# Performance work log

Hardware: AMD Instinct MI355X
Metric: run time of the kernel (lower is better)

## Reference

```python
import jax, jax.numpy as jnp
import numpy as np

EPS = 1e-8  # torch cosine_similarity norm clamp

def _cos(a, b, axis=-1):
    na = jnp.maximum(jnp.linalg.norm(a, axis=axis), EPS)
    nb = jnp.maximum(jnp.linalg.norm(b, axis=axis), EPS)
    return jnp.sum(a * b, axis=axis) / (na * nb)

def setup_inputs() -> dict:
    key = jax.random.key(0)
    ks = jax.random.split(key, 9)
    B, L, D, S = 8, 8192, 512, 131072
    scale = 0.02
    x = jax.random.normal(ks[0], (B, L, D), jnp.float32)
    context_W = jax.random.normal(ks[1], (D, D), jnp.float32) * scale
    context_b = jnp.zeros((D,), jnp.float32)
    pred_W1 = jax.random.normal(ks[2], (D, D), jnp.float32) * scale
    pred_b1 = jnp.zeros((D,), jnp.float32)
    pred_W2 = jax.random.normal(ks[3], (D, D), jnp.float32) * scale
    pred_b2 = jnp.zeros((D,), jnp.float32)
    raw_embeddings = jax.random.normal(ks[4], (S, D), jnp.float32)
    u = jax.random.uniform(ks[5], (S,), jnp.float32)
    surprise_level = jnp.where(u > 0.5, u, 0.0)  # ~half the slots active
    return {"x": x, "context_W": context_W, "context_b": context_b,
            "pred_W1": pred_W1, "pred_b1": pred_b1,
            "pred_W2": pred_W2, "pred_b2": pred_b2,
            "raw_embeddings": raw_embeddings, "surprise_level": surprise_level}

def reference(x, context_W, context_b, pred_W1, pred_b1, pred_W2, pred_b2,
              raw_embeddings, surprise_level):
    # context = pad(x[:, :-1], left-shift by one along seq), i.e. causal previous token
    context = jnp.pad(x[:, :-1, :], ((0, 0), (1, 0), (0, 0)))
    # predictor MLP on projected context (torch Linear: y = x @ W.T + b)
    ctx = context @ context_W.T + context_b
    h = jax.nn.gelu(ctx @ pred_W1.T + pred_b1, approximate=False)
    prediction = h @ pred_W2.T + pred_b2  # [B, L, D]
    mse = jnp.mean((x - prediction) ** 2, axis=-1)
    prediction_surprise = jnp.sqrt(mse)  # [B, L]

    # memory-contrastive surprise: cosine sim of pooled x vs active stored embeddings
    active = surprise_level > 0  # [S]
    x_pooled = jnp.mean(x, axis=1)  # [B, D]
    sim = _cos(x_pooled[:, None, :], raw_embeddings[None, :, :])  # [B, S]
    sim = jnp.where(active[None, :], sim, -jnp.inf)
    max_sim = jnp.max(sim, axis=-1)           # [B]
    best_idx = jnp.argmax(sim, axis=-1)       # [B]
    best_stored = raw_embeddings[best_idx]    # [B, D] argmax-based gather
    divergence = 1.0 - _cos(x, best_stored[:, None, :])  # [B, L]
    pattern_match = (max_sim[:, None] > 0.3).astype(x.dtype)
    contrastive = pattern_match * divergence

    surprise = jnp.maximum(prediction_surprise, contrastive * 2.0)  # [B, L]
    return surprise
```

## Files before the change

### kernel.cpp

```cpp
#include <hip/hip_runtime.h>
#include <math.h>

#define OFF_SIMKEY   0
#define OFF_POOLED   1024
#define OFF_SSD      32768
#define OFF_NX2      294912
#define OFF_DOT      557056
#define ZEROED_BYTES 819200
#define OFF_MAXSIM   819200
#define OFF_NORME    819456
#define OFF_EBEST    819712
#define OFF_BPRIME   836608
#define OFF_WP       839680
#define OFF_W2B      1364992
#define OFF_H        1900544

typedef __attribute__((ext_vector_type(8))) short bf16x8;
typedef __attribute__((ext_vector_type(4))) float f32x4;

__device__ inline unsigned short f2bf(float f) {
    unsigned int u = __float_as_uint(f);
    unsigned int r = (u + 0x7FFFu + ((u >> 16) & 1u)) >> 16;
    return (unsigned short)r;
}

__device__ inline void load_lds_16(const void* g, void* l) {
    __builtin_amdgcn_global_load_lds((const __attribute__((address_space(1))) void*)g,
                                     (__attribute__((address_space(3))) void*)l, 16, 0, 0);
}

__global__ void __launch_bounds__(256) k_pre(const float* __restrict__ W1, const float* __restrict__ Wc,
                      const float* __restrict__ b1, const float* __restrict__ bc,
                      unsigned short* __restrict__ Wp, float* __restrict__ bprime) {
    __shared__ float w1s[8 * 512];
    int t = threadIdx.x;
    int n0 = blockIdx.x * 8;
    const float4* src = (const float4*)(W1 + (size_t)n0 * 512);
    float4* dst = (float4*)w1s;
#pragma unroll
    for (int c = 0; c < 4; ++c) dst[t + c * 256] = src[t + c * 256];
    __syncthreads();
    int k0 = t, k1 = t + 256;
    float acc0[8], acc1[8];
#pragma unroll
    for (int n = 0; n < 8; ++n) { acc0[n] = 0.f; acc1[n] = 0.f; }
    for (int j = 0; j < 512; ++j) {
        float a = Wc[(size_t)j * 512 + k0];
        float b = Wc[(size_t)j * 512 + k1];
#pragma unroll
        for (int n = 0; n < 8; ++n) {
            float w = w1s[n * 512 + j];
            acc0[n] += w * a; acc1[n] += w * b;
        }
    }
#pragma unroll
    for (int n = 0; n < 8; ++n) {
        Wp[(size_t)(n0 + n) * 512 + k0] = f2bf(acc0[n]);
        Wp[(size_t)(n0 + n) * 512 + k1] = f2bf(acc1[n]);
    }
    int nl = t >> 5, l32 = t & 31;
    float p = 0.f;
    for (int j = l32; j < 512; j += 32) p += w1s[nl * 512 + j] * bc[j];
#pragma unroll
    for (int m = 16; m >= 1; m >>= 1) p += __shfl_xor(p, m);
    if (l32 == 0) bprime[n0 + nl] = b1[n0 + nl] + p;
}

__global__ void __launch_bounds__(256) k_cast(const float* __restrict__ W2, unsigned short* __restrict__ W2b) {
    int i = blockIdx.x * 1024 + threadIdx.x * 4;
    float4 v = *(const float4*)(W2 + i);
    ushort4 o;
    o.x = f2bf(v.x); o.y = f2bf(v.y); o.z = f2bf(v.z); o.w = f2bf(v.w);
    *(ushort4*)(W2b + i) = o;
}

__global__ void __launch_bounds__(512) k_pool(const float* __restrict__ x, float* __restrict__ pooled) {
    int d = threadIdx.x;
    int b = blockIdx.y;
    int l0 = blockIdx.x * 128;
    const float* p = x + ((size_t)b * 8192 + l0) * 512 + d;
    float s = 0.f;
    for (int i = 0; i < 128; ++i) s += p[(size_t)i * 512];
    atomicAdd(&pooled[b * 512 + d], s);
}

__global__ void __launch_bounds__(256) k_sim(const float* __restrict__ E, const float* __restrict__ sl,
                     const float* __restrict__ pooledws, unsigned long long* __restrict__ simkey) {
    __shared__ float ps[4096];
    __shared__ unsigned long long wkey[4][8];
    int t = threadIdx.x, lane = t & 63, w = t >> 6;
#pragma unroll
    for (int c = 0; c < 16; ++c) ps[t + c * 256] = pooledws[t + c * 256] * (1.0f / 8192.0f);
    __syncthreads();
    float pr[8][8];
#pragma unroll
    for (int b = 0; b < 8; ++b) {
        float4 v0 = *(const float4*)&ps[b * 512 + lane * 8];
        float4 v1 = *(const float4*)&ps[b * 512 + lane * 8 + 4];
        pr[b][0] = v0.x; pr[b][1] = v0.y; pr[b][2] = v0.z; pr[b][3] = v0.w;
        pr[b][4] = v1.x; pr[b][5] = v1.y; pr[b][6] = v1.z; pr[b][7] = v1.w;
    }
    float npinv[8];
#pragma unroll
    for (int b = 0; b < 8; ++b) {
        float s = 0.f;
#pragma unroll
        for (int j = 0; j < 8; ++j) s += pr[b][j] * pr[b][j];
#pragma unroll
        for (int m = 32; m >= 1; m >>= 1) s += __shfl_xor(s, m);
        npinv[b] = 1.0f / fmaxf(sqrtf(s), 1e-8f);
    }
    unsigned long long best[8];
#pragma unroll
    for (int b = 0; b < 8; ++b) best[b] = 0ull;
    int sbase = blockIdx.x * 512 + w * 128;
    for (int g = 0; g < 2; ++g) {
        float mysl = sl[sbase + g * 64 + lane];
        unsigned long long mask = __ballot(mysl > 0.0f);
        for (int it = 0; it < 64; ++it) {
            if (!((mask >> it) & 1ull)) continue;
            int s = sbase + g * 64 + it;
            const float4* ep = (const float4*)(E + (size_t)s * 512);
            float4 e0 = ep[lane * 2], e1 = ep[lane * 2 + 1];
            float nrm = e0.x * e0.x + e0.y * e0.y + e0.z * e0.z + e0.w * e0.w
                      + e1.x * e1.x + e1.y * e1.y + e1.z * e1.z + e1.w * e1.w;
            float dt[8];
#pragma unroll
            for (int b = 0; b < 8; ++b)
                dt[b] = e0.x * pr[b][0] + e0.y * pr[b][1] + e0.z * pr[b][2] + e0.w * pr[b][3]
                      + e1.x * pr[b][4] + e1.y * pr[b][5] + e1.z * pr[b][6] + e1.w * pr[b][7];
#pragma unroll
            for (int m = 32; m >= 1; m >>= 1) {
                nrm += __shfl_xor(nrm, m);
#pragma unroll
                for (int b = 0; b < 8; ++b) dt[b] += __shfl_xor(dt[b], m);
            }
            float neinv = 1.0f / fmaxf(sqrtf(nrm), 1e-8f);
#pragma unroll
            for (int b = 0; b < 8; ++b) {
                float sim = dt[b] * npinv[b] * neinv;
                unsigned int u = __float_as_uint(sim);
                unsigned int k32 = (u & 0x80000000u) ? ~u : (u | 0x80000000u);
                unsigned long long key = ((unsigned long long)k32 << 32) | (unsigned int)(~(unsigned int)s);
                if (key > best[b]) best[b] = key;
            }
        }
    }
    if (lane == 0) {
#pragma unroll
        for (int b = 0; b < 8; ++b) wkey[w][b] = best[b];
    }
    __syncthreads();
    if (t < 8) {
        unsigned long long k = wkey[0][t];
#pragma unroll
        for (int w2 = 1; w2 < 4; ++w2) if (wkey[w2][t] > k) k = wkey[w2][t];
        if (k) atomicMax(&simkey[t], k);
    }
}

__global__ void __launch_bounds__(64) k_b2(const float* __restrict__ E, const unsigned long long* __restrict__ simkey,
                    float* __restrict__ max_sim, float* __restrict__ norm_e, float* __restrict__ ebest) {
    int b = blockIdx.x, lane = threadIdx.x;
    unsigned long long key = simkey[b];
    float ms; unsigned int idx;
    if (key == 0ull) { ms = -1e30f; idx = 0u; }
    else {
        unsigned int k32 = (unsigned int)(key >> 32);
        unsigned int u = (k32 & 0x80000000u) ? (k32 & 0x7FFFFFFFu) : ~k32;
        ms = __uint_as_float(u);
        idx = ~(unsigned int)(key & 0xFFFFFFFFull);
    }
    const float4* ep = (const float4*)(E + (size_t)idx * 512);
    float4 e0 = ep[lane * 2], e1 = ep[lane * 2 + 1];
    *(float4*)&ebest[b * 512 + lane * 8] = e0;
    *(float4*)&ebest[b * 512 + lane * 8 + 4] = e1;
    float s = e0.x * e0.x + e0.y * e0.y + e0.z * e0.z + e0.w * e0.w
            + e1.x * e1.x + e1.y * e1.y + e1.z * e1.z + e1.w * e1.w;
#pragma unroll
    for (int m = 32; m >= 1; m >>= 1) s += __shfl_xor(s, m);
    if (lane == 0) { max_sim[b] = ms; norm_e[b] = fmaxf(sqrtf(s), 1e-8f); }
}

__global__ void __launch_bounds__(256) k_gemm1(const float* __restrict__ x, const unsigned short* __restrict__ Wp,
                        const float* __restrict__ bprime, unsigned short* __restrict__ H) {
    __shared__ char smem[32768];
    unsigned short* As = (unsigned short*)smem;
    unsigned short* Bs = (unsigned short*)(smem + 8192);
    int t = threadIdx.x, lane = t & 63, w = t >> 6, l15 = lane & 15, quad = lane >> 4;
    int cb = blockIdx.x, rb = blockIdx.y;
    int wr = w >> 1, wc = w & 1;
    f32x4 acc[4][4];
#pragma unroll
    for (int i = 0; i < 4; ++i)
#pragma unroll
        for (int j = 0; j < 4; ++j) acc[i][j] = (f32x4){0.f, 0.f, 0.f, 0.f};
    const int gr0 = rb * 128;
    for (int kt = 0; kt < 16; ++kt) {
        __syncthreads();
#pragma unroll
        for (int c = 0; c < 4; ++c) {
            int u = c * 256 + t;
            int row = u >> 3, f4 = u & 7;
            int gr = gr0 + row;
            int l = gr & 8191;
            float4 v = make_float4(0.f, 0.f, 0.f, 0.f);
            if (l != 0) v = *(const float4*)(x + ((size_t)gr - 1) * 512 + kt * 32 + f4 * 4);
            ushort4 o;
            o.x = f2bf(v.x); o.y = f2bf(v.y); o.z = f2bf(v.z); o.w = f2bf(v.w);
            *(ushort4*)&As[row * 32 + f4 * 4] = o;
        }
#pragma unroll
        for (int c = 0; c < 2; ++c) {
            int q = w * 2 + c;
            int unit = q * 64 + lane;
            int row = unit >> 2, kb = unit & 3;
            const unsigned short* g = Wp + (size_t)(cb * 128 + row) * 512 + kt * 32 + kb * 8;
            load_lds_16(g, Bs + q * 512);
        }
        __syncthreads();
        bf16x8 af[4], bfr[4];
#pragma unroll
        for (int i = 0; i < 4; ++i)
            af[i] = *(const bf16x8*)&As[(wr * 64 + i * 16 + l15) * 32 + quad * 8];
#pragma unroll
        for (int j = 0; j < 4; ++j)
            bfr[j] = *(const bf16x8*)&Bs[(wc * 64 + j * 16 + l15) * 32 + quad * 8];
#pragma unroll
        for (int i = 0; i < 4; ++i)
#pragma unroll
            for (int j = 0; j < 4; ++j)
                acc[i][j] = __builtin_amdgcn_mfma_f32_16x16x32_bf16(af[i], bfr[j], acc[i][j], 0, 0, 0);
    }
    __syncthreads();
    float bpj[4];
#pragma unroll
    for (int j = 0; j < 4; ++j) bpj[j] = bprime[cb * 128 + wc * 64 + j * 16 + l15];
    unsigned short* hs = (unsigned short*)smem;
#pragma unroll
    for (int i = 0; i < 4; ++i)
#pragma unroll
        for (int j = 0; j < 4; ++j)
#pragma unroll
            for (int r = 0; r < 4; ++r) {
                int m = wr * 64 + i * 16 + quad * 4 + r;
                int n = wc * 64 + j * 16 + l15;
                float v = acc[i][j][r] + bpj[j];
                v = 0.5f * v * (1.0f + erff(v * 0.70710678118f));
                hs[m * 128 + n] = f2bf(v);
            }
    __syncthreads();
    {
        int row = t >> 1, half = t & 1;
        const uint4* srcp = (const uint4*)(smem + row * 256 + half * 128);
        uint4* dstp = (uint4*)((char*)H + ((size_t)(gr0 + row)) * 1024 + cb * 256 + half * 128);
#pragma unroll
        for (int u2 = 0; u2 < 8; ++u2) dstp[u2] = srcp[u2];
    }
}

__global__ void __launch_bounds__(256) k_gemm2(const unsigned short* __restrict__ H, const unsigned short* __restrict__ W2b,
                        const float* __restrict__ b2, const float* __restrict__ x,
                        const float* __restrict__ ebest,
                        float* __restrict__ ssd, float* __restrict__ nx2, float* __restrict__ xdot) {
    __shared__ char smem[16384];
    unsigned short* As = (unsigned short*)smem;
    unsigned short* Bs = (unsigned short*)(smem + 8192);
    int t = threadIdx.x, lane = t & 63, w = t >> 6, l15 = lane & 15, quad = lane >> 4;
    int cb = blockIdx.x, rb = blockIdx.y;
    int wr = w >> 1, wc = w & 1;
    f32x4 acc[4][4];
#pragma unroll
    for (int i = 0; i < 4; ++i)
#pragma unroll
        for (int j = 0; j < 4; ++j) acc[i][j] = (f32x4){0.f, 0.f, 0.f, 0.f};
    const int gr0 = rb * 128;
    for (int kt = 0; kt < 16; ++kt) {
        __syncthreads();
#pragma unroll
        for (int c = 0; c < 2; ++c) {
            int q = w * 2 + c;
            int unit = q * 64 + lane;
            int row = unit >> 2, kb = unit & 3;
            const unsigned short* gA = H + (size_t)(gr0 + row) * 512 + kt * 32 + kb * 8;
            load_lds_16(gA, As + q * 512);
            const unsigned short* gB = W2b + (size_t)(cb * 128 + row) * 512 + kt * 32 + kb * 8;
            load_lds_16(gB, Bs + q * 512);
        }
        __syncthreads();
        bf16x8 af[4], bfr[4];
#pragma unroll
        for (int i = 0; i < 4; ++i)
            af[i] = *(const bf16x8*)&As[(wr * 64 + i * 16 + l15) * 32 + quad * 8];
#pragma unroll
        for (int j = 0; j < 4; ++j)
            bfr[j] = *(const bf16x8*)&Bs[(wc * 64 + j * 16 + l15) * 32 + quad * 8];
#pragma unroll
        for (int i = 0; i < 4; ++i)
#pragma unroll
            for (int j = 0; j < 4; ++j)
                acc[i][j] = __builtin_amdgcn_mfma_f32_16x16x32_bf16(af[i], bfr[j], acc[i][j], 0, 0, 0);
    }
    int b = gr0 >> 13;
    float b2j[4], ej[4];
#pragma unroll
    for (int j = 0; j < 4; ++j) {
        int n = cb * 128 + wc * 64 + j * 16 + l15;
        b2j[j] = b2[n];
        ej[j] = ebest[b * 512 + n];
    }
#pragma unroll
    for (int i = 0; i < 4; ++i)
#pragma unroll
        for (int r = 0; r < 4; ++r) {
            int gr = gr0 + wr * 64 + i * 16 + quad * 4 + r;
            float sd = 0.f, sx = 0.f, sdt = 0.f;
#pragma unroll
            for (int j = 0; j < 4; ++j) {
                int n = cb * 128 + wc * 64 + j * 16 + l15;
                float p = acc[i][j][r] + b2j[j];
                float xv = x[(size_t)gr * 512 + n];
                float d = xv - p;
                sd += d * d; sx += xv * xv; sdt += xv * ej[j];
            }
#pragma unroll
            for (int m = 8; m >= 1; m >>= 1) {
                sd += __shfl_xor(sd, m);
                sx += __shfl_xor(sx, m);
                sdt += __shfl_xor(sdt, m);
            }
            if (l15 == 0) {
                atomicAdd(&ssd[gr], sd);
                atomicAdd(&nx2[gr], sx);
                atomicAdd(&xdot[gr], sdt);
            }
        }
}

__global__ void __launch_bounds__(256) k_final(const float* __restrict__ ssd, const float* __restrict__ nx2,
                        const float* __restrict__ xdot, const float* __restrict__ max_sim,
                        const float* __restrict__ norm_e, float* __restrict__ out) {
    int r = blockIdx.x * 256 + threadIdx.x;
    int b = r >> 13;
    float ps = sqrtf(ssd[r] * (1.0f / 512.0f));
    float ms = max_sim[b];
    float c = 0.0f;
    if (ms > 0.3f) {
        float nx = fmaxf(sqrtf(nx2[r]), 1e-8f);
        float cs = xdot[r] / (nx * norm_e[b]);
        c = 2.0f * (1.0f - cs);
    }
    out[r] = fmaxf(ps, c);
}

extern "C" void kernel_launch(void* const* d_in, const int* in_sizes, int n_in,
                              void* d_out, int out_size, void* d_ws, size_t ws_size,
                              hipStream_t stream) {
    const float* x  = (const float*)d_in[0];
    const float* Wc = (const float*)d_in[1];
    const float* bc = (const float*)d_in[2];
    const float* W1 = (const float*)d_in[3];
    const float* b1 = (const float*)d_in[4];
    const float* W2 = (const float*)d_in[5];
    const float* b2 = (const float*)d_in[6];
    const float* E  = (const float*)d_in[7];
    const float* sl = (const float*)d_in[8];

    char* ws = (char*)d_ws;
    unsigned long long* simkey = (unsigned long long*)(ws + OFF_SIMKEY);
    float* pooled  = (float*)(ws + OFF_POOLED);
    float* ssd     = (float*)(ws + OFF_SSD);
    float* nx2     = (float*)(ws + OFF_NX2);
    float* xdot    = (float*)(ws + OFF_DOT);
    float* max_sim = (float*)(ws + OFF_MAXSIM);
    float* norm_e  = (float*)(ws + OFF_NORME);
    float* ebest   = (float*)(ws + OFF_EBEST);
    float* bprime  = (float*)(ws + OFF_BPRIME);
    unsigned short* Wp  = (unsigned short*)(ws + OFF_WP);
    unsigned short* W2b = (unsigned short*)(ws + OFF_W2B);
    unsigned short* H   = (unsigned short*)(ws + OFF_H);
    float* out = (float*)d_out;

    hipMemsetAsync(ws, 0, ZEROED_BYTES, stream);
    k_pre<<<64, 256, 0, stream>>>(W1, Wc, b1, bc, Wp, bprime);
    k_cast<<<256, 256, 0, stream>>>(W2, W2b);
    k_pool<<<dim3(64, 8), 512, 0, stream>>>(x, pooled);
    k_sim<<<256, 256, 0, stream>>>(E, sl, pooled, simkey);
    k_b2<<<8, 64, 0, stream>>>(E, simkey, max_sim, norm_e, ebest);
    k_gemm1<<<dim3(4, 512), 256, 0, stream>>>(x, Wp, bprime, H);
    k_gemm2<<<dim3(4, 512), 256, 0, stream>>>(H, W2b, b2, x, ebest, ssd, nx2, xdot);
    k_final<<<256, 256, 0, stream>>>(ssd, nx2, xdot, max_sim, norm_e, out);
}
```

Measured before the change: 812.3 us.

## Fuse both MLP GEMMs and finalization into one kernel, widen small kernels

Merges the two GEMM kernels and the final reduction into one kernel that processes 64 rows per block. The hidden activations stay in registers and LDS instead of making a round trip through global memory. Per-row reductions are done in LDS rather than with global atomics. k_pre and k_sim are also split across many more blocks to increase parallelism. The cost is more register pressure from holding the A and H tiles in registers, and the weight tiles are re-streamed for every 64-row block.

After: 793.4 us. -2.3%, faster.

```diff
diff --git a/kernel.cpp b/kernel.cpp
--- a/kernel.cpp
+++ b/kernel.cpp
@@ -3,17 +3,13 @@
 
 #define OFF_SIMKEY   0
 #define OFF_POOLED   1024
-#define OFF_SSD      32768
-#define OFF_NX2      294912
-#define OFF_DOT      557056
-#define ZEROED_BYTES 819200
-#define OFF_MAXSIM   819200
-#define OFF_NORME    819456
-#define OFF_EBEST    819712
-#define OFF_BPRIME   836608
-#define OFF_WP       839680
-#define OFF_W2B      1364992
-#define OFF_H        1900544
+#define ZEROED_BYTES 17408
+#define OFF_MAXSIM   17408
+#define OFF_NORME    17664
+#define OFF_EBEST    17920
+#define OFF_BPRIME   34304
+#define OFF_WP       36864
+#define OFF_W2B      561152
 
 typedef __attribute__((ext_vector_type(8))) short bf16x8;
 typedef __attribute__((ext_vector_type(4))) float f32x4;
@@ -32,38 +28,25 @@
 __global__ void __launch_bounds__(256) k_pre(const float* __restrict__ W1, const float* __restrict__ Wc,
                       const float* __restrict__ b1, const float* __restrict__ bc,
                       unsigned short* __restrict__ Wp, float* __restrict__ bprime) {
-    __shared__ float w1s[8 * 512];
+    __shared__ float w1row[512];
+    __shared__ float wsum[4];
     int t = threadIdx.x;
-    int n0 = blockIdx.x * 8;
-    const float4* src = (const float4*)(W1 + (size_t)n0 * 512);
-    float4* dst = (float4*)w1s;
-#pragma unroll
-    for (int c = 0; c < 4; ++c) dst[t + c * 256] = src[t + c * 256];
+    int n = blockIdx.x >> 1, half = blockIdx.x & 1;
+    if (t < 128) ((float4*)w1row)[t] = ((const float4*)(W1 + (size_t)n * 512))[t];
     __syncthreads();
-    int k0 = t, k1 = t + 256;
-    float acc0[8], acc1[8];
-#pragma unroll
-    for (int n = 0; n < 8; ++n) { acc0[n] = 0.f; acc1[n] = 0.f; }
-    for (int j = 0; j < 512; ++j) {
-        float a = Wc[(size_t)j * 512 + k0];
-        float b = Wc[(size_t)j * 512 + k1];
-#pragma unroll
-        for (int n = 0; n < 8; ++n) {
-            float w = w1s[n * 512 + j];
-            acc0[n] += w * a; acc1[n] += w * b;
-        }
-    }
-#pragma unroll
-    for (int n = 0; n < 8; ++n) {
-        Wp[(size_t)(n0 + n) * 512 + k0] = f2bf(acc0[n]);
-        Wp[(size_t)(n0 + n) * 512 + k1] = f2bf(acc1[n]);
-    }
-    int nl = t >> 5, l32 = t & 31;
-    float p = 0.f;
-    for (int j = l32; j < 512; j += 32) p += w1s[nl * 512 + j] * bc[j];
-#pragma unroll
-    for (int m = 16; m >= 1; m >>= 1) p += __shfl_xor(p, m);
-    if (l32 == 0) bprime[n0 + nl] = b1[n0 + nl] + p;
+    int k = half * 256 + t;
+    float acc = 0.f;
+#pragma unroll 8
+    for (int j = 0; j < 512; ++j) acc += w1row[j] * Wc[(size_t)j * 512 + k];
+    Wp[(size_t)n * 512 + k] = f2bf(acc);
+    if (half == 0) {
+        float p = w1row[t] * bc[t] + w1row[t + 256] * bc[t + 256];
+#pragma unroll
+        for (int m = 32; m >= 1; m >>= 1) p += __shfl_xor(p, m);
+        if ((t & 63) == 0) wsum[t >> 6] = p;
+        __syncthreads();
+        if (t == 0) bprime[n] = b1[n] + wsum[0] + wsum[1] + wsum[2] + wsum[3];
+    }
 }
 
 __global__ void __launch_bounds__(256) k_cast(const float* __restrict__ W2, unsigned short* __restrict__ W2b) {
@@ -113,37 +96,35 @@
     unsigned long long best[8];
 #pragma unroll
     for (int b = 0; b < 8; ++b) best[b] = 0ull;
-    int sbase = blockIdx.x * 512 + w * 128;
-    for (int g = 0; g < 2; ++g) {
-        float mysl = sl[sbase + g * 64 + lane];
-        unsigned long long mask = __ballot(mysl > 0.0f);
-        for (int it = 0; it < 64; ++it) {
-            if (!((mask >> it) & 1ull)) continue;
-            int s = sbase + g * 64 + it;
-            const float4* ep = (const float4*)(E + (size_t)s * 512);
-            float4 e0 = ep[lane * 2], e1 = ep[lane * 2 + 1];
-            float nrm = e0.x * e0.x + e0.y * e0.y + e0.z * e0.z + e0.w * e0.w
-                      + e1.x * e1.x + e1.y * e1.y + e1.z * e1.z + e1.w * e1.w;
-            float dt[8];
-#pragma unroll
-            for (int b = 0; b < 8; ++b)
-                dt[b] = e0.x * pr[b][0] + e0.y * pr[b][1] + e0.z * pr[b][2] + e0.w * pr[b][3]
-                      + e1.x * pr[b][4] + e1.y * pr[b][5] + e1.z * pr[b][6] + e1.w * pr[b][7];
-#pragma unroll
-            for (int m = 32; m >= 1; m >>= 1) {
-                nrm += __shfl_xor(nrm, m);
-#pragma unroll
-                for (int b = 0; b < 8; ++b) dt[b] += __shfl_xor(dt[b], m);
-            }
-            float neinv = 1.0f / fmaxf(sqrtf(nrm), 1e-8f);
-#pragma unroll
-            for (int b = 0; b < 8; ++b) {
-                float sim = dt[b] * npinv[b] * neinv;
-                unsigned int u = __float_as_uint(sim);
-                unsigned int k32 = (u & 0x80000000u) ? ~u : (u | 0x80000000u);
-                unsigned long long key = ((unsigned long long)k32 << 32) | (unsigned int)(~(unsigned int)s);
-                if (key > best[b]) best[b] = key;
-            }
+    int sbase = blockIdx.x * 64 + w * 16;
+    float mysl = (lane < 16) ? sl[sbase + lane] : 0.f;
+    unsigned long long mask = __ballot(mysl > 0.0f);
+    for (int it = 0; it < 16; ++it) {
+        if (!((mask >> it) & 1ull)) continue;
+        int s = sbase + it;
+        const float4* ep = (const float4*)(E + (size_t)s * 512);
+        float4 e0 = ep[lane * 2], e1 = ep[lane * 2 + 1];
+        float nrm = e0.x * e0.x + e0.y * e0.y + e0.z * e0.z + e0.w * e0.w
+                  + e1.x * e1.x + e1.y * e1.y + e1.z * e1.z + e1.w * e1.w;
+        float dt[8];
+#pragma unroll
+        for (int b = 0; b < 8; ++b)
+            dt[b] = e0.x * pr[b][0] + e0.y * pr[b][1] + e0.z * pr[b][2] + e0.w * pr[b][3]
+                  + e1.x * pr[b][4] + e1.y * pr[b][5] + e1.z * pr[b][6] + e1.w * pr[b][7];
+#pragma unroll
+        for (int m = 32; m >= 1; m >>= 1) {
+            nrm += __shfl_xor(nrm, m);
+#pragma unroll
+            for (int b = 0; b < 8; ++b) dt[b] += __shfl_xor(dt[b], m);
+        }
+        float neinv = 1.0f / fmaxf(sqrtf(nrm), 1e-8f);
+#pragma unroll
+        for (int b = 0; b < 8; ++b) {
+            float sim = dt[b] * npinv[b] * neinv;
+            unsigned int u = __float_as_uint(sim);
+            unsigned int k32 = (u & 0x80000000u) ? ~u : (u | 0x80000000u);
+            unsigned long long key = ((unsigned long long)k32 << 32) | (unsigned int)(~(unsigned int)s);
+            if (key > best[b]) best[b] = key;
         }
     }
     if (lane == 0) {
@@ -182,147 +163,159 @@
     if (lane == 0) { max_sim[b] = ms; norm_e[b] = fmaxf(sqrtf(s), 1e-8f); }
 }
 
-__global__ void __launch_bounds__(256) k_gemm1(const float* __restrict__ x, const unsigned short* __restrict__ Wp,
-                        const float* __restrict__ bprime, unsigned short* __restrict__ H) {
+__global__ void __launch_bounds__(256, 2) k_fused(
+        const float* __restrict__ x, const unsigned short* __restrict__ Wp,
+        const float* __restrict__ bprime, const unsigned short* __restrict__ W2b,
+        const float* __restrict__ b2, const float* __restrict__ ebest,
+        const float* __restrict__ max_sim, const float* __restrict__ norm_e,
+        float* __restrict__ out) {
     __shared__ char smem[32768];
-    unsigned short* As = (unsigned short*)smem;
-    unsigned short* Bs = (unsigned short*)(smem + 8192);
+    unsigned short* Ts   = (unsigned short*)smem;
+    unsigned short* Bs   = (unsigned short*)(smem + 5120);
+    unsigned short* hbuf = (unsigned short*)(smem + 13312);
+    float* red           = (float*)(smem + 30720);
     int t = threadIdx.x, lane = t & 63, w = t >> 6, l15 = lane & 15, quad = lane >> 4;
-    int cb = blockIdx.x, rb = blockIdx.y;
     int wr = w >> 1, wc = w & 1;
-    f32x4 acc[4][4];
-#pragma unroll
-    for (int i = 0; i < 4; ++i)
-#pragma unroll
-        for (int j = 0; j < 4; ++j) acc[i][j] = (f32x4){0.f, 0.f, 0.f, 0.f};
-    const int gr0 = rb * 128;
-    for (int kt = 0; kt < 16; ++kt) {
-        __syncthreads();
-#pragma unroll
-        for (int c = 0; c < 4; ++c) {
-            int u = c * 256 + t;
-            int row = u >> 3, f4 = u & 7;
-            int gr = gr0 + row;
-            int l = gr & 8191;
+    const int gr0 = blockIdx.x * 64;
+    const int b = gr0 >> 13;
+    const int row0 = t >> 3, f4 = t & 7;
+
+    ushort4 ush[16][2];
+#pragma unroll
+    for (int c = 0; c < 2; ++c) {
+        int gr = gr0 + row0 + c * 32;
+        bool z = ((gr & 8191) == 0);
+        const float* src = x + ((size_t)gr - 1) * 512 + f4 * 4;
+#pragma unroll
+        for (int kt = 0; kt < 16; ++kt) {
             float4 v = make_float4(0.f, 0.f, 0.f, 0.f);
-            if (l != 0) v = *(const float4*)(x + ((size_t)gr - 1) * 512 + kt * 32 + f4 * 4);
+            if (!z) v = *(const float4*)(src + kt * 32);
             ushort4 o;
             o.x = f2bf(v.x); o.y = f2bf(v.y); o.z = f2bf(v.z); o.w = f2bf(v.w);
-            *(ushort4*)&As[row * 32 + f4 * 4] = o;
-        }
-#pragma unroll
-        for (int c = 0; c < 2; ++c) {
-            int q = w * 2 + c;
-            int unit = q * 64 + lane;
-            int row = unit >> 2, kb = unit & 3;
-            const unsigned short* g = Wp + (size_t)(cb * 128 + row) * 512 + kt * 32 + kb * 8;
-            load_lds_16(g, Bs + q * 512);
-        }
+            ush[kt][c] = o;
+        }
+    }
+
+    ushort4 hregs[16][2];
+#pragma unroll
+    for (int cb = 0; cb < 4; ++cb) {
+        f32x4 acc[2][4];
+#pragma unroll
+        for (int i = 0; i < 2; ++i)
+#pragma unroll
+            for (int j = 0; j < 4; ++j) acc[i][j] = (f32x4){0.f, 0.f, 0.f, 0.f};
+#pragma unroll
+        for (int kt = 0; kt < 16; ++kt) {
+            __syncthreads();
+            *(ushort4*)&Ts[row0 * 40 + f4 * 4]        = ush[kt][0];
+            *(ushort4*)&Ts[(row0 + 32) * 40 + f4 * 4] = ush[kt][1];
+#pragma unroll
+            for (int c = 0; c < 2; ++c) {
+                int unit = c * 256 + w * 64 + lane;
+                int row = unit >> 2, kb = unit & 3;
+                load_lds_16(Wp + (size_t)(cb * 128 + row) * 512 + kt * 32 + kb * 8,
+                            Bs + (size_t)(c * 256 + w * 64) * 8);
+            }
+            __syncthreads();
+            bf16x8 af[2], bfr[4];
+            af[0] = *(const bf16x8*)&Ts[(wr * 32 + l15) * 40 + quad * 8];
+            af[1] = *(const bf16x8*)&Ts[(wr * 32 + 16 + l15) * 40 + quad * 8];
+#pragma unroll
+            for (int j = 0; j < 4; ++j)
+                bfr[j] = *(const bf16x8*)&Bs[(wc * 64 + j * 16 + l15) * 32 + quad * 8];
+#pragma unroll
+            for (int i = 0; i < 2; ++i)
+#pragma unroll
+                for (int j = 0; j < 4; ++j)
+                    acc[i][j] = __builtin_amdgcn_mfma_f32_16x16x32_bf16(af[i], bfr[j], acc[i][j], 0, 0, 0);
+        }
+        float bpj[4];
+#pragma unroll
+        for (int j = 0; j < 4; ++j) bpj[j] = bprime[cb * 128 + wc * 64 + j * 16 + l15];
+#pragma unroll
+        for (int i = 0; i < 2; ++i)
+#pragma unroll
+            for (int j = 0; j < 4; ++j)
+#pragma unroll
+                for (int r = 0; r < 4; ++r) {
+                    int m = wr * 32 + i * 16 + quad * 4 + r;
+                    int n = wc * 64 + j * 16 + l15;
+                    float v = acc[i][j][r] + bpj[j];
+                    v = 0.5f * v * (1.0f + erff(v * 0.70710678118f));
+                    hbuf[m * 136 + n] = f2bf(v);
+                }
         __syncthreads();
-        bf16x8 af[4], bfr[4];
-#pragma unroll
-        for (int i = 0; i < 4; ++i)
-            af[i] = *(const bf16x8*)&As[(wr * 64 + i * 16 + l15) * 32 + quad * 8];
-#pragma unroll
-        for (int j = 0; j < 4; ++j)
-            bfr[j] = *(const bf16x8*)&Bs[(wc * 64 + j * 16 + l15) * 32 + quad * 8];
-#pragma unroll
-        for (int i = 0; i < 4; ++i)
+#pragma unroll
+        for (int ktl = 0; ktl < 4; ++ktl) {
+            hregs[cb * 4 + ktl][0] = *(const ushort4*)&hbuf[row0 * 136 + ktl * 32 + f4 * 4];
+            hregs[cb * 4 + ktl][1] = *(const ushort4*)&hbuf[(row0 + 32) * 136 + ktl * 32 + f4 * 4];
+        }
+    }
+
+    float psd[2][4], psx[2][4], pdt[2][4];
+#pragma unroll
+    for (int i = 0; i < 2; ++i)
+#pragma unroll
+        for (int r = 0; r < 4; ++r) { psd[i][r] = 0.f; psx[i][r] = 0.f; pdt[i][r] = 0.f; }
+#pragma unroll
+    for (int cb2 = 0; cb2 < 4; ++cb2) {
+        f32x4 acc[2][4];
+#pragma unroll
+        for (int i = 0; i < 2; ++i)
+#pragma unroll
+            for (int j = 0; j < 4; ++j) acc[i][j] = (f32x4){0.f, 0.f, 0.f, 0.f};
+#pragma unroll
+        for (int kt = 0; kt < 16; ++kt) {
+            __syncthreads();
+            *(ushort4*)&Ts[row0 * 40 + f4 * 4]        = hregs[kt][0];
+            *(ushort4*)&Ts[(row0 + 32) * 40 + f4 * 4] = hregs[kt][1];
+#pragma unroll
+            for (int c = 0; c < 2; ++c) {
+                int unit = c * 256 + w * 64 + lane;
+                int row = unit >> 2, kb = unit & 3;
+                load_lds_16(W2b + (size_t)(cb2 * 128 + row) * 512 + kt * 32 + kb * 8,
+                            Bs + (size_t)(c * 256 + w * 64) * 8);
+            }
+            __syncthreads();
+            bf16x8 af[2], bfr[4];
+            af[0] = *(const bf16x8*)&Ts[(wr * 32 + l15) * 40 + quad * 8];
+            af[1] = *(const bf16x8*)&Ts[(wr * 32 + 16 + l15) * 40 + quad * 8];
 #pragma unroll
             for (int j = 0; j < 4; ++j)
-                acc[i][j] = __builtin_amdgcn_mfma_f32_16x16x32_bf16(af[i], bfr[j], acc[i][j], 0, 0, 0);
-    }
-    __syncthreads();
-    float bpj[4];
-#pragma unroll
-    for (int j = 0; j < 4; ++j) bpj[j] = bprime[cb * 128 + wc * 64 + j * 16 + l15];
-    unsigned short* hs = (unsigned short*)smem;
-#pragma unroll
-    for (int i = 0; i < 4; ++i)
-#pragma unroll
-        for (int j = 0; j < 4; ++j)
+                bfr[j] = *(const bf16x8*)&Bs[(wc * 64 + j * 16 + l15) * 32 + quad * 8];
+#pragma unroll
+            for (int i = 0; i < 2; ++i)
+#pragma unroll
+                for (int j = 0; j < 4; ++j)
+                    acc[i][j] = __builtin_amdgcn_mfma_f32_16x16x32_bf16(af[i], bfr[j], acc[i][j], 0, 0, 0);
+        }
+        float b2j[4], ej[4];
+#pragma unroll
+        for (int j = 0; j < 4; ++j) {
+            int n = cb2 * 128 + wc * 64 + j * 16 + l15;
+            b2j[j] = b2[n];
+            ej[j] = ebest[b * 512 + n];
+        }
+#pragma unroll
+        for (int i = 0; i < 2; ++i)
 #pragma unroll
             for (int r = 0; r < 4; ++r) {
-                int m = wr * 64 + i * 16 + quad * 4 + r;
-                int n = wc * 64 + j * 16 + l15;
-                float v = acc[i][j][r] + bpj[j];
-                v = 0.5f * v * (1.0f + erff(v * 0.70710678118f));
-                hs[m * 128 + n] = f2bf(v);
-            }
-    __syncthreads();
-    {
-        int row = t >> 1, half = t & 1;
-        const uint4* srcp = (const uint4*)(smem + row * 256 + half * 128);
-        uint4* dstp = (uint4*)((char*)H + ((size_t)(gr0 + row)) * 1024 + cb * 256 + half * 128);
-#pragma unroll
-        for (int u2 = 0; u2 < 8; ++u2) dstp[u2] = srcp[u2];
-    }
-}
-
-__global__ void __launch_bounds__(256) k_gemm2(const unsigned short* __restrict__ H, const unsigned short* __restrict__ W2b,
-                        const float* __restrict__ b2, const float* __restrict__ x,
-                        const float* __restrict__ ebest,
-                        float* __restrict__ ssd, float* __restrict__ nx2, float* __restrict__ xdot) {
-    __shared__ char smem[16384];
-    unsigned short* As = (unsigned short*)smem;
-    unsigned short* Bs = (unsigned short*)(smem + 8192);
-    int t = threadIdx.x, lane = t & 63, w = t >> 6, l15 = lane & 15, quad = lane >> 4;
-    int cb = blockIdx.x, rb = blockIdx.y;
-    int wr = w >> 1, wc = w & 1;
-    f32x4 acc[4][4];
-#pragma unroll
-    for (int i = 0; i < 4; ++i)
-#pragma unroll
-        for (int j = 0; j < 4; ++j) acc[i][j] = (f32x4){0.f, 0.f, 0.f, 0.f};
-    const int gr0 = rb * 128;
-    for (int kt = 0; kt < 16; ++kt) {
-        __syncthreads();
-#pragma unroll
-        for (int c = 0; c < 2; ++c) {
-            int q = w * 2 + c;
-            int unit = q * 64 + lane;
-            int row = unit >> 2, kb = unit & 3;
-            const unsigned short* gA = H + (size_t)(gr0 + row) * 512 + kt * 32 + kb * 8;
-            load_lds_16(gA, As + q * 512);
-            const unsigned short* gB = W2b + (size_t)(cb * 128 + row) * 512 + kt * 32 + kb * 8;
-            load_lds_16(gB, Bs + q * 512);
-        }
-        __syncthreads();
-        bf16x8 af[4], bfr[4];
-#pragma unroll
-        for (int i = 0; i < 4; ++i)
-            af[i] = *(const bf16x8*)&As[(wr * 64 + i * 16 + l15) * 32 + quad * 8];
-#pragma unroll
-        for (int j = 0; j < 4; ++j)
-            bfr[j] = *(const bf16x8*)&Bs[(wc * 64 + j * 16 + l15) * 32 + quad * 8];
-#pragma unroll
-        for (int i = 0; i < 4; ++i)
-#pragma unroll
-            for (int j = 0; j < 4; ++j)
-                acc[i][j] = __builtin_amdgcn_mfma_f32_16x16x32_bf16(af[i], bfr[j], acc[i][j], 0, 0, 0);
-    }
-    int b = gr0 >> 13;
-    float b2j[4], ej[4];
-#pragma unroll
-    for (int j = 0; j < 4; ++j) {
-        int n = cb * 128 + wc * 64 + j * 16 + l15;
-        b2j[j] = b2[n];
-        ej[j] = ebest[b * 512 + n];
-    }
-#pragma unroll
-    for (int i = 0; i < 4; ++i)
+                int gr = gr0 + wr * 32 + i * 16 + quad * 4 + r;
+#pragma unroll
+                for (int j = 0; j < 4; ++j) {
+                    int n = cb2 * 128 + wc * 64 + j * 16 + l15;
+                    float p = acc[i][j][r] + b2j[j];
+                    float xv = x[(size_t)gr * 512 + n];
+                    float d = xv - p;
+                    psd[i][r] += d * d; psx[i][r] += xv * xv; pdt[i][r] += xv * ej[j];
+                }
+            }
+    }
+#pragma unroll
+    for (int i = 0; i < 2; ++i)
 #pragma unroll
         for (int r = 0; r < 4; ++r) {
-            int gr = gr0 + wr * 64 + i * 16 + quad * 4 + r;
-            float sd = 0.f, sx = 0.f, sdt = 0.f;
-#pragma unroll
-            for (int j = 0; j < 4; ++j) {
-                int n = cb * 128 + wc * 64 + j * 16 + l15;
-                float p = acc[i][j][r] + b2j[j];
-                float xv = x[(size_t)gr * 512 + n];
-                float d = xv - p;
-                sd += d * d; sx += xv * xv; sdt += xv * ej[j];
-            }
+            float sd = psd[i][r], sx = psx[i][r], sdt = pdt[i][r];
 #pragma unroll
             for (int m = 8; m >= 1; m >>= 1) {
                 sd += __shfl_xor(sd, m);
@@ -330,27 +323,28 @@
                 sdt += __shfl_xor(sdt, m);
             }
             if (l15 == 0) {
-                atomicAdd(&ssd[gr], sd);
-                atomicAdd(&nx2[gr], sx);
-                atomicAdd(&xdot[gr], sdt);
-            }
-        }
-}
-
-__global__ void __launch_bounds__(256) k_final(const float* __restrict__ ssd, const float* __restrict__ nx2,
-                        const float* __restrict__ xdot, const float* __restrict__ max_sim,
-                        const float* __restrict__ norm_e, float* __restrict__ out) {
-    int r = blockIdx.x * 256 + threadIdx.x;
-    int b = r >> 13;
-    float ps = sqrtf(ssd[r] * (1.0f / 512.0f));
-    float ms = max_sim[b];
-    float c = 0.0f;
-    if (ms > 0.3f) {
-        float nx = fmaxf(sqrtf(nx2[r]), 1e-8f);
-        float cs = xdot[r] / (nx * norm_e[b]);
-        c = 2.0f * (1.0f - cs);
-    }
-    out[r] = fmaxf(ps, c);
+                int rl = i * 16 + quad * 4 + r;
+                red[(w * 32 + rl) * 4 + 0] = sd;
+                red[(w * 32 + rl) * 4 + 1] = sx;
+                red[(w * 32 + rl) * 4 + 2] = sdt;
+            }
+        }
+    __syncthreads();
+    if (t < 64) {
+        int rl = t & 31;
+        int base = (t >> 5) * 2;
+        float sd  = red[((base) * 32 + rl) * 4 + 0] + red[((base + 1) * 32 + rl) * 4 + 0];
+        float sx  = red[((base) * 32 + rl) * 4 + 1] + red[((base + 1) * 32 + rl) * 4 + 1];
+        float sdt = red[((base) * 32 + rl) * 4 + 2] + red[((base + 1) * 32 + rl) * 4 + 2];
+        float ps = sqrtf(sd * (1.0f / 512.0f));
+        float ms = max_sim[b];
+        float c = 0.f;
+        if (ms > 0.3f) {
+            float nx = fmaxf(sqrtf(sx), 1e-8f);
+            c = 2.0f * (1.0f - sdt / (nx * norm_e[b]));
+        }
+        out[gr0 + t] = fmaxf(ps, c);
+    }
 }
 
 extern "C" void kernel_launch(void* const* d_in, const int* in_sizes, int n_in,
@@ -369,25 +363,19 @@
     char* ws = (char*)d_ws;
     unsigned long long* simkey = (unsigned long long*)(ws + OFF_SIMKEY);
     float* pooled  = (float*)(ws + OFF_POOLED);
-    float* ssd     = (float*)(ws + OFF_SSD);
-    float* nx2     = (float*)(ws + OFF_NX2);
-    float* xdot    = (float*)(ws + OFF_DOT);
     float* max_sim = (float*)(ws + OFF_MAXSIM);
     float* norm_e  = (float*)(ws + OFF_NORME);
     float* ebest   = (float*)(ws + OFF_EBEST);
     float* bprime  = (float*)(ws + OFF_BPRIME);
     unsigned short* Wp  = (unsigned short*)(ws + OFF_WP);
     unsigned short* W2b = (unsigned short*)(ws + OFF_W2B);
-    unsigned short* H   = (unsigned short*)(ws + OFF_H);
     float* out = (float*)d_out;
 
     hipMemsetAsync(ws, 0, ZEROED_BYTES, stream);
-    k_pre<<<64, 256, 0, stream>>>(W1, Wc, b1, bc, Wp, bprime);
+    k_pre<<<1024, 256, 0, stream>>>(W1, Wc, b1, bc, Wp, bprime);
     k_cast<<<256, 256, 0, stream>>>(W2, W2b);
     k_pool<<<dim3(64, 8), 512, 0, stream>>>(x, pooled);
-    k_sim<<<256, 256, 0, stream>>>(E, sl, pooled, simkey);
+    k_sim<<<2048, 256, 0, stream>>>(E, sl, pooled, simkey);
     k_b2<<<8, 64, 0, stream>>>(E, simkey, max_sim, norm_e, ebest);
-    k_gemm1<<<dim3(4, 512), 256, 0, stream>>>(x, Wp, bprime, H);
-    k_gemm2<<<dim3(4, 512), 256, 0, stream>>>(H, W2b, b2, x, ebest, ssd, nx2, xdot);
-    k_final<<<256, 256, 0, stream>>>(ssd, nx2, xdot, max_sim, norm_e, out);
-}
+    k_fused<<<1024, 256, 0, stream>>>(x, Wp, bprime, W2b, b2, ebest, max_sim, norm_e, out);
+}
```
